# Kernel optimization log

Hardware: AMD Instinct MI355X
Metric: run time of the kernel (lower is better)

Reference implementation:

```python
import jax, jax.numpy as jnp
import numpy as np

N_NODES = 500000


def _gcn_conv(x, W, b, src, dst, n):
    # x: [N, Fin], W: [Fin, Fout]. PyG GCNConv with add_self_loops + sym norm.
    h = x @ W                                            # [N, Fout]
    deg = jax.ops.segment_sum(jnp.ones_like(dst, dtype=h.dtype), dst,
                              num_segments=n)            # in-degree incl self loops
    dinv = jnp.where(deg > 0, jax.lax.rsqrt(jnp.maximum(deg, 1)), 0.0)
    norm = dinv[src] * dinv[dst]                         # [E]
    msg = h[src] * norm[:, None]                         # gather + scale
    out = jax.ops.segment_sum(msg, dst, num_segments=n)  # scatter-add to targets
    return out + b


def setup_inputs() -> dict:
    key = jax.random.key(0)
    k1, k2, k3, k4 = jax.random.split(key, 4)
    x = jax.random.normal(k1, (N_NODES, 1), dtype=jnp.float32)
    edge_index = jax.random.randint(k2, (2, 8000000), 0, N_NODES, dtype=jnp.int64)
    W1 = jax.random.normal(k3, (1, 32), dtype=jnp.float32) * (1.0 / np.sqrt(1))
    b1 = jnp.zeros((32,), dtype=jnp.float32)
    W2 = jax.random.normal(k4, (32, 2), dtype=jnp.float32) * (1.0 / np.sqrt(32))
    b2 = jnp.zeros((2,), dtype=jnp.float32)
    return {"x": x, "edge_index": edge_index, "W1": W1, "b1": b1, "W2": W2, "b2": b2}


def reference(x, edge_index, W1, b1, W2, b2):
    n = x.shape[0]
    loops = jnp.arange(n, dtype=edge_index.dtype)
    src = jnp.concatenate([edge_index[0], loops])  # add self-loops
    dst = jnp.concatenate([edge_index[1], loops])
    h = _gcn_conv(x, W1, b1, src, dst, n)
    h = jax.nn.relu(h)
    # F.dropout(training=self.training): identity in eval mode
    h = _gcn_conv(h, W2, b2, src, dst, n)
    return jax.nn.log_softmax(h, axis=1)
```

## Files before the change

### kernel.cpp

```cpp
#include <hip/hip_runtime.h>


static constexpr int BKT_BITS = 11;
static constexpr int BKT = 1 << BKT_BITS;
static constexpr int NB = 256;
static constexpr int HB = 512;
static constexpr int HT = 256;
static constexpr int CHUNK = 8192;
static constexpr int SCT = 256;
static constexpr int PERT = CHUNK / SCT;

__global__ void __launch_bounds__(HT) k_hist(const int* __restrict__ dst, int e,
                                             int chunk, int nbkt,
                                             unsigned* __restrict__ totals) {
  __shared__ unsigned cnt[NB];
  for (int t = threadIdx.x; t < NB; t += HT) cnt[t] = 0;
  __syncthreads();
  int lo = blockIdx.x * chunk;
  int hi = min(lo + chunk, e);
  const int4* d4 = (const int4*)dst;
  for (int i = (lo >> 2) + threadIdx.x; i < (hi >> 2); i += HT) {
    int4 d = d4[i];
    atomicAdd(&cnt[((unsigned)d.x) >> BKT_BITS], 1u);
    atomicAdd(&cnt[((unsigned)d.y) >> BKT_BITS], 1u);
    atomicAdd(&cnt[((unsigned)d.z) >> BKT_BITS], 1u);
    atomicAdd(&cnt[((unsigned)d.w) >> BKT_BITS], 1u);
  }
  for (int i = ((hi >> 2) << 2) + threadIdx.x; i < hi; i += HT)
    atomicAdd(&cnt[((unsigned)dst[i]) >> BKT_BITS], 1u);
  __syncthreads();
  for (int t = threadIdx.x; t < nbkt; t += HT)
    if (cnt[t]) atomicAdd(&totals[t], cnt[t]);
}

__global__ void k_basescan(const unsigned* __restrict__ totals, int nbkt,
                           unsigned* __restrict__ gcur) {
  int lane = threadIdx.x;
  unsigned running = 0;
  for (int c = 0; c < NB; c += 64) {
    int k = c + lane;
    unsigned v = (k < nbkt) ? totals[k] : 0u;
    unsigned incl = v;
#pragma unroll
    for (int off = 1; off < 64; off <<= 1) {
      unsigned t = __shfl_up(incl, off);
      if (lane >= off) incl += t;
    }
    if (k < nbkt) gcur[k] = running + incl - v;
    running += __shfl(incl, 63);
  }
}

__global__ void __launch_bounds__(SCT) k_scatter(
    const int* __restrict__ src, const int* __restrict__ dst, int e, int nbkt,
    unsigned* __restrict__ gcur, unsigned* __restrict__ packed) {
  __shared__ unsigned staged[CHUNK];
  __shared__ unsigned cnt[NB];
  __shared__ unsigned cur[NB];
  __shared__ unsigned gseg[NB];
  __shared__ unsigned loff[NB + 1];
  const int tid = threadIdx.x;
  const int lo = blockIdx.x * CHUNK;
  for (int t = tid; t < NB; t += SCT) { cnt[t] = 0u; cur[t] = 0u; }
  __syncthreads();

  unsigned pk[PERT];
  unsigned bku[PERT / 4];
  const int4* s4 = (const int4*)src;
  const int4* d4 = (const int4*)dst;
#pragma unroll
  for (int jj = 0; jj < PERT / 4; ++jj) {
    int i4 = (lo >> 2) + jj * SCT + tid;
    unsigned b4 = 0xFFFFFFFFu;
    if (i4 * 4 + 3 < e) {
      int4 s = s4[i4];
      int4 d = d4[i4];
      unsigned k0 = ((unsigned)d.x) >> BKT_BITS, k1 = ((unsigned)d.y) >> BKT_BITS;
      unsigned k2 = ((unsigned)d.z) >> BKT_BITS, k3 = ((unsigned)d.w) >> BKT_BITS;
      pk[jj * 4 + 0] = ((unsigned)s.x << BKT_BITS) | ((unsigned)d.x & (BKT - 1));
      pk[jj * 4 + 1] = ((unsigned)s.y << BKT_BITS) | ((unsigned)d.y & (BKT - 1));
      pk[jj * 4 + 2] = ((unsigned)s.z << BKT_BITS) | ((unsigned)d.z & (BKT - 1));
      pk[jj * 4 + 3] = ((unsigned)s.w << BKT_BITS) | ((unsigned)d.w & (BKT - 1));
      b4 = k0 | (k1 << 8) | (k2 << 16) | (k3 << 24);
      atomicAdd(&cnt[k0], 1u);
      atomicAdd(&cnt[k1], 1u);
      atomicAdd(&cnt[k2], 1u);
      atomicAdd(&cnt[k3], 1u);
    } else {
#pragma unroll
      for (int c = 0; c < 4; ++c) {
        int i = i4 * 4 + c;
        if (i >= lo && i < e) {
          unsigned dd = (unsigned)dst[i];
          unsigned kk = dd >> BKT_BITS;
          pk[jj * 4 + c] = ((unsigned)src[i] << BKT_BITS) | (dd & (BKT - 1));
          b4 = (b4 & ~(0xFFu << (8 * c))) | (kk << (8 * c));
          atomicAdd(&cnt[kk], 1u);
        }
      }
    }
    bku[jj] = b4;
  }
  __syncthreads();

  if (tid < 64) {
    unsigned running = 0;
    for (int c = 0; c < NB; c += 64) {
      int k = c + tid;
      unsigned v = cnt[k];
      unsigned incl = v;
#pragma unroll
      for (int off = 1; off < 64; off <<= 1) {
        unsigned t = __shfl_up(incl, off);
        if (tid >= off) incl += t;
      }
      loff[k] = running + incl - v;
      running += __shfl(incl, 63);
    }
    if (tid == 0) loff[NB] = running;
  }
  __syncthreads();

  for (int k = tid; k < nbkt; k += SCT)
    if (cnt[k]) gseg[k] = atomicAdd(&gcur[k], cnt[k]);

#pragma unroll
  for (int jj = 0; jj < PERT / 4; ++jj) {
    unsigned b4 = bku[jj];
#pragma unroll
    for (int c = 0; c < 4; ++c) {
      unsigned k = (b4 >> (8 * c)) & 0xFFu;
      if (k != 0xFFu) {
        unsigned pos = loff[k] + atomicAdd(&cur[k], 1u);
        staged[pos] = pk[jj * 4 + c];
      }
    }
  }
  __syncthreads();

  int mv = (int)loff[nbkt];
  for (int t = tid; t < mv; t += SCT) {
    int a = 0, b = nbkt;
    while (b - a > 1) {
      int mid = (a + b) >> 1;
      if ((int)loff[mid] <= t) a = mid; else b = mid;
    }
    packed[gseg[a] + (unsigned)(t - (int)loff[a])] = staged[t];
  }
}

__global__ void __launch_bounds__(1024) k_degnode(
    const unsigned* __restrict__ packed, const unsigned* __restrict__ gcur,
    const float* __restrict__ x, int n, float* __restrict__ dinv,
    float* __restrict__ xs) {
  __shared__ unsigned cnt[BKT];
  int k = blockIdx.x;
  for (int t = threadIdx.x; t < BKT; t += blockDim.x) cnt[t] = 0;
  __syncthreads();
  unsigned lo = k ? gcur[k - 1] : 0u, hi = gcur[k];
  for (unsigned i = lo + threadIdx.x; i < hi; i += blockDim.x)
    atomicAdd(&cnt[packed[i] & (BKT - 1)], 1u);
  __syncthreads();
  int g0 = k << BKT_BITS;
  for (int t = threadIdx.x; t < BKT; t += blockDim.x) {
    int g = g0 + t;
    if (g < n) {
      float di = rsqrtf((float)(cnt[t] + 1u));
      dinv[g] = di;
      xs[g] = di * x[g];
    }
  }
}

__global__ void __launch_bounds__(1024) k_accA2(
    const unsigned* __restrict__ packed, const unsigned* __restrict__ gcur,
    const float* __restrict__ dinv, const float* __restrict__ xs,
    const float* __restrict__ W1, const float* __restrict__ b1,
    const float* __restrict__ W2, int n, float2* __restrict__ yd) {
  __shared__ float acc[BKT];
  __shared__ float sW1[32], sb1[32], sW2[64];
  if (threadIdx.x < 32) {
    sW1[threadIdx.x] = W1[threadIdx.x];
    sb1[threadIdx.x] = b1[threadIdx.x];
  } else if (threadIdx.x < 96) {
    sW2[threadIdx.x - 32] = W2[threadIdx.x - 32];
  }
  for (int t = threadIdx.x; t < BKT; t += blockDim.x) acc[t] = 0.0f;
  __syncthreads();
  int k = blockIdx.x;
  unsigned lo = k ? gcur[k - 1] : 0u, hi = gcur[k];
  for (unsigned i = lo + threadIdx.x; i < hi; i += blockDim.x) {
    unsigned p = packed[i];
    atomicAdd(&acc[p & (BKT - 1)], xs[p >> BKT_BITS]);
  }
  __syncthreads();
  int g0 = k << BKT_BITS;
  for (int t = threadIdx.x; t < BKT; t += blockDim.x) {
    int g = g0 + t;
    if (g >= n) continue;
    float di = dinv[g];
    float s = di * (acc[t] + xs[g]);
    float y0 = 0.0f, y1 = 0.0f;
#pragma unroll
    for (int f = 0; f < 32; ++f) {
      float h = fmaxf(fmaf(s, sW1[f], sb1[f]), 0.0f);
      y0 = fmaf(h, sW2[2 * f + 0], y0);
      y1 = fmaf(h, sW2[2 * f + 1], y1);
    }
    yd[g] = make_float2(di * y0, di * y1);
  }
}

__global__ void __launch_bounds__(1024) k_accB3(
    const unsigned* __restrict__ packed, const unsigned* __restrict__ gcur,
    const float* __restrict__ dinv, const float2* __restrict__ yd,
    const float* __restrict__ b2, int n, float2* __restrict__ out) {
  __shared__ float a0[BKT], a1[BKT];
  for (int t = threadIdx.x; t < BKT; t += blockDim.x) {
    a0[t] = 0.0f;
    a1[t] = 0.0f;
  }
  __syncthreads();
  int k = blockIdx.x;
  unsigned lo = k ? gcur[k - 1] : 0u, hi = gcur[k];
  for (unsigned i = lo + threadIdx.x; i < hi; i += blockDim.x) {
    unsigned p = packed[i];
    float2 v = yd[p >> BKT_BITS];
    unsigned l = p & (BKT - 1);
    atomicAdd(&a0[l], v.x);
    atomicAdd(&a1[l], v.y);
  }
  __syncthreads();
  float b20 = b2[0], b21 = b2[1];
  int g0 = k << BKT_BITS;
  for (int t = threadIdx.x; t < BKT; t += blockDim.x) {
    int g = g0 + t;
    if (g >= n) continue;
    float di = dinv[g];
    float2 yv = yd[g];
    float t0 = fmaf(di, a0[t] + yv.x, b2[0] * 0.0f + b20);
    float t1 = fmaf(di, a1[t] + yv.y, b21);
    float m = fmaxf(t0, t1);
    float l2 = m + logf(expf(t0 - m) + expf(t1 - m));
    out[g] = make_float2(t0 - l2, t1 - l2);
  }
}

extern "C" void kernel_launch(void* const* d_in, const int* in_sizes, int n_in,
                              void* d_out, int out_size, void* d_ws, size_t ws_size,
                              hipStream_t stream) {
  const float* x = (const float*)d_in[0];
  const int* edge = (const int*)d_in[1];
  const float* W1 = (const float*)d_in[2];
  const float* b1 = (const float*)d_in[3];
  const float* W2 = (const float*)d_in[4];
  const float* b2 = (const float*)d_in[5];
  float2* out = (float2*)d_out;

  const int n = in_sizes[0];
  const int e = in_sizes[1] / 2;
  const int* src = edge;
  const int* dst = edge + e;

  const int nbkt = (n + BKT - 1) >> BKT_BITS;
  const int hchunk = (((e + HB - 1) / HB) + 3) & ~3;
  const int sgrid = (e + CHUNK - 1) / CHUNK;

  char* ws = (char*)d_ws;
  unsigned* packed = (unsigned*)ws;
  unsigned* totals = (unsigned*)(ws + (size_t)e * 4);
  unsigned* gcur = totals + NB;
  float* dinv = (float*)(gcur + NB);
  float* xs = dinv + n;
  float2* yd = (float2*)(xs + n);

  hipMemsetAsync(totals, 0, NB * sizeof(unsigned), stream);
  k_hist<<<HB, HT, 0, stream>>>(dst, e, hchunk, nbkt, totals);
  k_basescan<<<1, 64, 0, stream>>>(totals, nbkt, gcur);
  k_scatter<<<sgrid, SCT, 0, stream>>>(src, dst, e, nbkt, gcur, packed);
  k_degnode<<<nbkt, 1024, 0, stream>>>(packed, gcur, x, n, dinv, xs);
  k_accA2<<<nbkt, 1024, 0, stream>>>(packed, gcur, dinv, xs, W1, b1, W2, n, yd);
  k_accB3<<<nbkt, 1024, 0, stream>>>(packed, gcur, dinv, yd, b2, n, out);
}
```

Before: 236.3 us.

## Split per-bucket accumulation across multiple blocks with partial sums and node kernels

Each destination bucket's edge range is now divided into S slices, each handled by a 256-thread block that writes a partial accumulator array to workspace. Separate per-node kernels then sum the partials and apply the dense MLP or log-softmax. The aim is more blocks per bucket, since about 245 buckets underfill the GPU's CUs. Loads are unrolled 4x, and nontemporal loads and stores are added on the packed edge stream. The cost is two extra launches plus workspace traffic for the partials, and S depends on the available workspace size.

```diff
diff --git a/kernel.cpp b/kernel.cpp
--- a/kernel.cpp
+++ b/kernel.cpp
@@ -9,6 +9,7 @@
 static constexpr int CHUNK = 8192;
 static constexpr int SCT = 256;
 static constexpr int PERT = CHUNK / SCT;
+static constexpr int AT = 256;
 
 __global__ void __launch_bounds__(HT) k_hist(const int* __restrict__ dst, int e,
                                              int chunk, int nbkt,
@@ -145,7 +146,8 @@
       int mid = (a + b) >> 1;
       if ((int)loff[mid] <= t) a = mid; else b = mid;
     }
-    packed[gseg[a] + (unsigned)(t - (int)loff[a])] = staged[t];
+    __builtin_nontemporal_store(staged[t],
+                                packed + gseg[a] + (unsigned)(t - (int)loff[a]));
   }
 }
 
@@ -155,14 +157,24 @@
     float* __restrict__ xs) {
   __shared__ unsigned cnt[BKT];
   int k = blockIdx.x;
-  for (int t = threadIdx.x; t < BKT; t += blockDim.x) cnt[t] = 0;
+  for (int t = threadIdx.x; t < BKT; t += 1024) cnt[t] = 0;
   __syncthreads();
   unsigned lo = k ? gcur[k - 1] : 0u, hi = gcur[k];
-  for (unsigned i = lo + threadIdx.x; i < hi; i += blockDim.x)
-    atomicAdd(&cnt[packed[i] & (BKT - 1)], 1u);
+  unsigned i = lo + threadIdx.x;
+  for (; i + 3u * 1024u < hi; i += 4096u) {
+    unsigned p0 = __builtin_nontemporal_load(packed + i);
+    unsigned p1 = __builtin_nontemporal_load(packed + i + 1024);
+    unsigned p2 = __builtin_nontemporal_load(packed + i + 2048);
+    unsigned p3 = __builtin_nontemporal_load(packed + i + 3072);
+    atomicAdd(&cnt[p0 & (BKT - 1)], 1u);
+    atomicAdd(&cnt[p1 & (BKT - 1)], 1u);
+    atomicAdd(&cnt[p2 & (BKT - 1)], 1u);
+    atomicAdd(&cnt[p3 & (BKT - 1)], 1u);
+  }
+  for (; i < hi; i += 1024u) atomicAdd(&cnt[packed[i] & (BKT - 1)], 1u);
   __syncthreads();
   int g0 = k << BKT_BITS;
-  for (int t = threadIdx.x; t < BKT; t += blockDim.x) {
+  for (int t = threadIdx.x; t < BKT; t += 1024) {
     int g = g0 + t;
     if (g < n) {
       float di = rsqrtf((float)(cnt[t] + 1u));
@@ -172,12 +184,49 @@
   }
 }
 
-__global__ void __launch_bounds__(1024) k_accA2(
+__global__ void __launch_bounds__(AT) k_accA_part(
     const unsigned* __restrict__ packed, const unsigned* __restrict__ gcur,
-    const float* __restrict__ dinv, const float* __restrict__ xs,
-    const float* __restrict__ W1, const float* __restrict__ b1,
-    const float* __restrict__ W2, int n, float2* __restrict__ yd) {
+    const float* __restrict__ xs, int S, float* __restrict__ pA) {
   __shared__ float acc[BKT];
+  int k = blockIdx.x / S, s = blockIdx.x - k * S;
+  for (int t = threadIdx.x; t < BKT; t += AT) acc[t] = 0.0f;
+  __syncthreads();
+  unsigned blo = k ? gcur[k - 1] : 0u, bhi = gcur[k];
+  unsigned slice = (bhi - blo + S - 1) / S;
+  unsigned lo = blo + s * slice;
+  unsigned hi = lo + slice;
+  if (hi > bhi) hi = bhi;
+  if (lo > bhi) lo = bhi;
+  unsigned i = lo + threadIdx.x;
+  for (; i + 3u * AT < hi; i += 4u * AT) {
+    unsigned p0 = __builtin_nontemporal_load(packed + i);
+    unsigned p1 = __builtin_nontemporal_load(packed + i + AT);
+    unsigned p2 = __builtin_nontemporal_load(packed + i + 2 * AT);
+    unsigned p3 = __builtin_nontemporal_load(packed + i + 3 * AT);
+    float v0 = xs[p0 >> BKT_BITS];
+    float v1 = xs[p1 >> BKT_BITS];
+    float v2 = xs[p2 >> BKT_BITS];
+    float v3 = xs[p3 >> BKT_BITS];
+    atomicAdd(&acc[p0 & (BKT - 1)], v0);
+    atomicAdd(&acc[p1 & (BKT - 1)], v1);
+    atomicAdd(&acc[p2 & (BKT - 1)], v2);
+    atomicAdd(&acc[p3 & (BKT - 1)], v3);
+  }
+  for (; i < hi; i += AT) {
+    unsigned p = packed[i];
+    atomicAdd(&acc[p & (BKT - 1)], xs[p >> BKT_BITS]);
+  }
+  __syncthreads();
+  float* dstp = pA + ((size_t)(k * S + s) << BKT_BITS);
+  for (int t = threadIdx.x; t < BKT; t += AT)
+    __builtin_nontemporal_store(acc[t], dstp + t);
+}
+
+__global__ void __launch_bounds__(256) k_nodeA(
+    const float* __restrict__ pA, const float* __restrict__ dinv,
+    const float* __restrict__ xs, const float* __restrict__ W1,
+    const float* __restrict__ b1, const float* __restrict__ W2, int S, int n,
+    float2* __restrict__ yd) {
   __shared__ float sW1[32], sb1[32], sW2[64];
   if (threadIdx.x < 32) {
     sW1[threadIdx.x] = W1[threadIdx.x];
@@ -185,65 +234,87 @@
   } else if (threadIdx.x < 96) {
     sW2[threadIdx.x - 32] = W2[threadIdx.x - 32];
   }
-  for (int t = threadIdx.x; t < BKT; t += blockDim.x) acc[t] = 0.0f;
-  __syncthreads();
-  int k = blockIdx.x;
-  unsigned lo = k ? gcur[k - 1] : 0u, hi = gcur[k];
-  for (unsigned i = lo + threadIdx.x; i < hi; i += blockDim.x) {
-    unsigned p = packed[i];
-    atomicAdd(&acc[p & (BKT - 1)], xs[p >> BKT_BITS]);
-  }
-  __syncthreads();
-  int g0 = k << BKT_BITS;
-  for (int t = threadIdx.x; t < BKT; t += blockDim.x) {
-    int g = g0 + t;
-    if (g >= n) continue;
-    float di = dinv[g];
-    float s = di * (acc[t] + xs[g]);
-    float y0 = 0.0f, y1 = 0.0f;
-#pragma unroll
-    for (int f = 0; f < 32; ++f) {
-      float h = fmaxf(fmaf(s, sW1[f], sb1[f]), 0.0f);
-      y0 = fmaf(h, sW2[2 * f + 0], y0);
-      y1 = fmaf(h, sW2[2 * f + 1], y1);
-    }
-    yd[g] = make_float2(di * y0, di * y1);
-  }
-}
-
-__global__ void __launch_bounds__(1024) k_accB3(
+  __syncthreads();
+  int g = blockIdx.x * 256 + threadIdx.x;
+  if (g >= n) return;
+  int k = g >> BKT_BITS, t = g & (BKT - 1);
+  float a = 0.0f;
+  for (int s = 0; s < S; ++s) a += pA[((size_t)(k * S + s) << BKT_BITS) + t];
+  float di = dinv[g];
+  float sv = di * (a + xs[g]);
+  float y0 = 0.0f, y1 = 0.0f;
+#pragma unroll
+  for (int f = 0; f < 32; ++f) {
+    float h = fmaxf(fmaf(sv, sW1[f], sb1[f]), 0.0f);
+    y0 = fmaf(h, sW2[2 * f + 0], y0);
+    y1 = fmaf(h, sW2[2 * f + 1], y1);
+  }
+  yd[g] = make_float2(di * y0, di * y1);
+}
+
+__global__ void __launch_bounds__(AT) k_accB_part(
     const unsigned* __restrict__ packed, const unsigned* __restrict__ gcur,
-    const float* __restrict__ dinv, const float2* __restrict__ yd,
-    const float* __restrict__ b2, int n, float2* __restrict__ out) {
-  __shared__ float a0[BKT], a1[BKT];
-  for (int t = threadIdx.x; t < BKT; t += blockDim.x) {
-    a0[t] = 0.0f;
-    a1[t] = 0.0f;
-  }
-  __syncthreads();
-  int k = blockIdx.x;
-  unsigned lo = k ? gcur[k - 1] : 0u, hi = gcur[k];
-  for (unsigned i = lo + threadIdx.x; i < hi; i += blockDim.x) {
+    const float2* __restrict__ yd, int S, float2* __restrict__ pB) {
+  __shared__ float2 av[BKT];
+  int k = blockIdx.x / S, s = blockIdx.x - k * S;
+  for (int t = threadIdx.x; t < BKT; t += AT) av[t] = make_float2(0.0f, 0.0f);
+  __syncthreads();
+  unsigned blo = k ? gcur[k - 1] : 0u, bhi = gcur[k];
+  unsigned slice = (bhi - blo + S - 1) / S;
+  unsigned lo = blo + s * slice;
+  unsigned hi = lo + slice;
+  if (hi > bhi) hi = bhi;
+  if (lo > bhi) lo = bhi;
+  unsigned i = lo + threadIdx.x;
+  for (; i + 3u * AT < hi; i += 4u * AT) {
+    unsigned p0 = __builtin_nontemporal_load(packed + i);
+    unsigned p1 = __builtin_nontemporal_load(packed + i + AT);
+    unsigned p2 = __builtin_nontemporal_load(packed + i + 2 * AT);
+    unsigned p3 = __builtin_nontemporal_load(packed + i + 3 * AT);
+    float2 v0 = yd[p0 >> BKT_BITS];
+    float2 v1 = yd[p1 >> BKT_BITS];
+    float2 v2 = yd[p2 >> BKT_BITS];
+    float2 v3 = yd[p3 >> BKT_BITS];
+    atomicAdd(&av[p0 & (BKT - 1)].x, v0.x);
+    atomicAdd(&av[p0 & (BKT - 1)].y, v0.y);
+    atomicAdd(&av[p1 & (BKT - 1)].x, v1.x);
+    atomicAdd(&av[p1 & (BKT - 1)].y, v1.y);
+    atomicAdd(&av[p2 & (BKT - 1)].x, v2.x);
+    atomicAdd(&av[p2 & (BKT - 1)].y, v2.y);
+    atomicAdd(&av[p3 & (BKT - 1)].x, v3.x);
+    atomicAdd(&av[p3 & (BKT - 1)].y, v3.y);
+  }
+  for (; i < hi; i += AT) {
     unsigned p = packed[i];
     float2 v = yd[p >> BKT_BITS];
-    unsigned l = p & (BKT - 1);
-    atomicAdd(&a0[l], v.x);
-    atomicAdd(&a1[l], v.y);
-  }
-  __syncthreads();
-  float b20 = b2[0], b21 = b2[1];
-  int g0 = k << BKT_BITS;
-  for (int t = threadIdx.x; t < BKT; t += blockDim.x) {
-    int g = g0 + t;
-    if (g >= n) continue;
-    float di = dinv[g];
-    float2 yv = yd[g];
-    float t0 = fmaf(di, a0[t] + yv.x, b2[0] * 0.0f + b20);
-    float t1 = fmaf(di, a1[t] + yv.y, b21);
-    float m = fmaxf(t0, t1);
-    float l2 = m + logf(expf(t0 - m) + expf(t1 - m));
-    out[g] = make_float2(t0 - l2, t1 - l2);
-  }
+    atomicAdd(&av[p & (BKT - 1)].x, v.x);
+    atomicAdd(&av[p & (BKT - 1)].y, v.y);
+  }
+  __syncthreads();
+  float2* dstp = pB + ((size_t)(k * S + s) << BKT_BITS);
+  for (int t = threadIdx.x; t < BKT; t += AT) dstp[t] = av[t];
+}
+
+__global__ void __launch_bounds__(256) k_nodeB(
+    const float2* __restrict__ pB, const float* __restrict__ dinv,
+    const float2* __restrict__ yd, const float* __restrict__ b2, int S, int n,
+    float2* __restrict__ out) {
+  int g = blockIdx.x * 256 + threadIdx.x;
+  if (g >= n) return;
+  int k = g >> BKT_BITS, t = g & (BKT - 1);
+  float s0 = 0.0f, s1 = 0.0f;
+  for (int s = 0; s < S; ++s) {
+    float2 v = pB[((size_t)(k * S + s) << BKT_BITS) + t];
+    s0 += v.x;
+    s1 += v.y;
+  }
+  float di = dinv[g];
+  float2 yv = yd[g];
+  float t0 = fmaf(di, s0 + yv.x, b2[0]);
+  float t1 = fmaf(di, s1 + yv.y, b2[1]);
+  float m = fmaxf(t0, t1);
+  float l = m + logf(expf(t0 - m) + expf(t1 - m));
+  out[g] = make_float2(t0 - l, t1 - l);
 }
 
 extern "C" void kernel_launch(void* const* d_in, const int* in_sizes, int n_in,
@@ -265,20 +336,31 @@
   const int nbkt = (n + BKT - 1) >> BKT_BITS;
   const int hchunk = (((e + HB - 1) / HB) + 3) & ~3;
   const int sgrid = (e + CHUNK - 1) / CHUNK;
+  const int ngrid = (n + 255) / 256;
 
   char* ws = (char*)d_ws;
-  unsigned* packed = (unsigned*)ws;
-  unsigned* totals = (unsigned*)(ws + (size_t)e * 4);
-  unsigned* gcur = totals + NB;
-  float* dinv = (float*)(gcur + NB);
-  float* xs = dinv + n;
-  float2* yd = (float2*)(xs + n);
+  size_t off = 0;
+  unsigned* packed = (unsigned*)(ws + off); off += (size_t)e * 4;
+  unsigned* totals = (unsigned*)(ws + off); off += NB * 4;
+  unsigned* gcur = (unsigned*)(ws + off);   off += NB * 4;
+  float* dinv = (float*)(ws + off);         off += (size_t)n * 4;
+  float* xs = (float*)(ws + off);           off += (size_t)n * 4;
+  float2* yd = (float2*)(ws + off);         off += (size_t)n * 8;
+  size_t rem = (ws_size > off) ? ws_size - off : 0;
+  int SA = (int)(rem / ((size_t)nbkt * BKT * 4));
+  int SB = (int)(rem / ((size_t)nbkt * BKT * 8));
+  SA = SA < 1 ? 1 : (SA > 8 ? 8 : SA);
+  SB = SB < 1 ? 1 : (SB > 8 ? 8 : SB);
+  float* pA = (float*)(ws + off);
+  float2* pB = (float2*)(ws + off);
 
   hipMemsetAsync(totals, 0, NB * sizeof(unsigned), stream);
   k_hist<<<HB, HT, 0, stream>>>(dst, e, hchunk, nbkt, totals);
   k_basescan<<<1, 64, 0, stream>>>(totals, nbkt, gcur);
   k_scatter<<<sgrid, SCT, 0, stream>>>(src, dst, e, nbkt, gcur, packed);
   k_degnode<<<nbkt, 1024, 0, stream>>>(packed, gcur, x, n, dinv, xs);
-  k_accA2<<<nbkt, 1024, 0, stream>>>(packed, gcur, dinv, xs, W1, b1, W2, n, yd);
-  k_accB3<<<nbkt, 1024, 0, stream>>>(packed, gcur, dinv, yd, b2, n, out);
-}
+  k_accA_part<<<nbkt * SA, AT, 0, stream>>>(packed, gcur, xs, SA, pA);
+  k_nodeA<<<ngrid, 256, 0, stream>>>(pA, dinv, xs, W1, b1, W2, SA, n, yd);
+  k_accB_part<<<nbkt * SB, AT, 0, stream>>>(packed, gcur, yd, SB, pB);
+  k_nodeB<<<ngrid, 256, 0, stream>>>(pB, dinv, yd, b2, SB, n, out);
+}
```

New measurement: 247.4 us. 1.05x slower.

## Sub-bin edges by source range with deterministic per-chunk scan offsets

Applied to the files above, without the earlier changes.

The bucketing of edges now uses a 2D bin (destination bucket × source range of 65536), so within each destination bucket the edges are ordered by source block. This should improve locality of the xs/yd gathers in the aggregation kernels. Global atomics for segment allocation are replaced by a per-chunk histogram, a column scan and a bin scan. The aggregation kernels also switch to 128-bit nontemporal loads of the packed edges, and the scatter uses nontemporal stores. The cost is a larger histogram workspace, an extra scan pass (nbin blocks), and more LDS per scatter block, which may lower occupancy.

```diff
diff --git a/kernel.cpp b/kernel.cpp
--- a/kernel.cpp
+++ b/kernel.cpp
@@ -3,109 +3,141 @@
 
 static constexpr int BKT_BITS = 11;
 static constexpr int BKT = 1 << BKT_BITS;
-static constexpr int NB = 256;
-static constexpr int HB = 512;
-static constexpr int HT = 256;
+static constexpr int SRC_SH = 16;
+static constexpr int NBIN_MAX = 2048;
 static constexpr int CHUNK = 8192;
 static constexpr int SCT = 256;
 static constexpr int PERT = CHUNK / SCT;
 
-__global__ void __launch_bounds__(HT) k_hist(const int* __restrict__ dst, int e,
-                                             int chunk, int nbkt,
-                                             unsigned* __restrict__ totals) {
-  __shared__ unsigned cnt[NB];
-  for (int t = threadIdx.x; t < NB; t += HT) cnt[t] = 0;
-  __syncthreads();
-  int lo = blockIdx.x * chunk;
-  int hi = min(lo + chunk, e);
+using u32x4 = __attribute__((ext_vector_type(4))) unsigned;
+
+__global__ void __launch_bounds__(SCT) k_hist(const int* __restrict__ src,
+                                              const int* __restrict__ dst, int e,
+                                              int nbin, int C,
+                                              unsigned* __restrict__ hist) {
+  __shared__ unsigned cnt[NBIN_MAX];
+  for (int t = threadIdx.x; t < NBIN_MAX; t += SCT) cnt[t] = 0;
+  __syncthreads();
+  int lo = blockIdx.x * CHUNK;
+  int hi = min(lo + CHUNK, e);
+  const int4* s4 = (const int4*)src;
   const int4* d4 = (const int4*)dst;
-  for (int i = (lo >> 2) + threadIdx.x; i < (hi >> 2); i += HT) {
+  for (int i = (lo >> 2) + threadIdx.x; i < (hi >> 2); i += SCT) {
+    int4 s = s4[i];
     int4 d = d4[i];
-    atomicAdd(&cnt[((unsigned)d.x) >> BKT_BITS], 1u);
-    atomicAdd(&cnt[((unsigned)d.y) >> BKT_BITS], 1u);
-    atomicAdd(&cnt[((unsigned)d.z) >> BKT_BITS], 1u);
-    atomicAdd(&cnt[((unsigned)d.w) >> BKT_BITS], 1u);
-  }
-  for (int i = ((hi >> 2) << 2) + threadIdx.x; i < hi; i += HT)
-    atomicAdd(&cnt[((unsigned)dst[i]) >> BKT_BITS], 1u);
-  __syncthreads();
-  for (int t = threadIdx.x; t < nbkt; t += HT)
-    if (cnt[t]) atomicAdd(&totals[t], cnt[t]);
-}
-
-__global__ void k_basescan(const unsigned* __restrict__ totals, int nbkt,
-                           unsigned* __restrict__ gcur) {
+    atomicAdd(&cnt[(((unsigned)d.x) >> BKT_BITS) * C + (((unsigned)s.x) >> SRC_SH)], 1u);
+    atomicAdd(&cnt[(((unsigned)d.y) >> BKT_BITS) * C + (((unsigned)s.y) >> SRC_SH)], 1u);
+    atomicAdd(&cnt[(((unsigned)d.z) >> BKT_BITS) * C + (((unsigned)s.z) >> SRC_SH)], 1u);
+    atomicAdd(&cnt[(((unsigned)d.w) >> BKT_BITS) * C + (((unsigned)s.w) >> SRC_SH)], 1u);
+  }
+  for (int i = ((hi >> 2) << 2) + threadIdx.x; i < hi; i += SCT)
+    atomicAdd(&cnt[(((unsigned)dst[i]) >> BKT_BITS) * C + (((unsigned)src[i]) >> SRC_SH)], 1u);
+  __syncthreads();
+  unsigned* hrow = hist + (size_t)blockIdx.x * nbin;
+  for (int t = threadIdx.x; t < nbin; t += SCT) hrow[t] = cnt[t];
+}
+
+__global__ void k_colscan(const unsigned* __restrict__ hist, int sgrid, int nbin,
+                          unsigned* __restrict__ colpre,
+                          unsigned* __restrict__ totals) {
+  int k = blockIdx.x;
   int lane = threadIdx.x;
   unsigned running = 0;
-  for (int c = 0; c < NB; c += 64) {
-    int k = c + lane;
-    unsigned v = (k < nbkt) ? totals[k] : 0u;
+  int rounds = (sgrid + 63) >> 6;
+  for (int c = 0; c < rounds; ++c) {
+    int b = c * 64 + lane;
+    unsigned v = (b < sgrid) ? hist[(size_t)b * nbin + k] : 0u;
     unsigned incl = v;
 #pragma unroll
     for (int off = 1; off < 64; off <<= 1) {
       unsigned t = __shfl_up(incl, off);
       if (lane >= off) incl += t;
     }
-    if (k < nbkt) gcur[k] = running + incl - v;
+    if (b < sgrid) colpre[(size_t)b * nbin + k] = running + incl - v;
     running += __shfl(incl, 63);
   }
+  if (lane == 0) totals[k] = running;
+}
+
+__global__ void k_binscan(const unsigned* __restrict__ totals, int nbin,
+                          unsigned* __restrict__ base) {
+  int lane = threadIdx.x;
+  unsigned running = 0;
+  for (int c = 0; c < NBIN_MAX; c += 64) {
+    int k = c + lane;
+    unsigned v = (k < nbin) ? totals[k] : 0u;
+    unsigned incl = v;
+#pragma unroll
+    for (int off = 1; off < 64; off <<= 1) {
+      unsigned t = __shfl_up(incl, off);
+      if (lane >= off) incl += t;
+    }
+    if (k < nbin) base[k] = running + incl - v;
+    running += __shfl(incl, 63);
+  }
+  if (lane == 0) base[nbin] = running;
 }
 
 __global__ void __launch_bounds__(SCT) k_scatter(
-    const int* __restrict__ src, const int* __restrict__ dst, int e, int nbkt,
-    unsigned* __restrict__ gcur, unsigned* __restrict__ packed) {
+    const int* __restrict__ src, const int* __restrict__ dst, int e, int nbin,
+    int C, const unsigned* __restrict__ colpre, const unsigned* __restrict__ base,
+    unsigned* __restrict__ packed) {
   __shared__ unsigned staged[CHUNK];
-  __shared__ unsigned cnt[NB];
-  __shared__ unsigned cur[NB];
-  __shared__ unsigned gseg[NB];
-  __shared__ unsigned loff[NB + 1];
+  __shared__ unsigned cnt[NBIN_MAX];
+  __shared__ unsigned loff[NBIN_MAX + 1];
+  __shared__ unsigned gbase[NBIN_MAX];
   const int tid = threadIdx.x;
   const int lo = blockIdx.x * CHUNK;
-  for (int t = tid; t < NB; t += SCT) { cnt[t] = 0u; cur[t] = 0u; }
+  for (int t = tid; t < NBIN_MAX; t += SCT) cnt[t] = 0u;
   __syncthreads();
 
   unsigned pk[PERT];
-  unsigned bku[PERT / 4];
+  unsigned short bin[PERT];
   const int4* s4 = (const int4*)src;
   const int4* d4 = (const int4*)dst;
 #pragma unroll
   for (int jj = 0; jj < PERT / 4; ++jj) {
     int i4 = (lo >> 2) + jj * SCT + tid;
-    unsigned b4 = 0xFFFFFFFFu;
     if (i4 * 4 + 3 < e) {
       int4 s = s4[i4];
       int4 d = d4[i4];
-      unsigned k0 = ((unsigned)d.x) >> BKT_BITS, k1 = ((unsigned)d.y) >> BKT_BITS;
-      unsigned k2 = ((unsigned)d.z) >> BKT_BITS, k3 = ((unsigned)d.w) >> BKT_BITS;
+      unsigned b0 = (((unsigned)d.x) >> BKT_BITS) * C + (((unsigned)s.x) >> SRC_SH);
+      unsigned b1 = (((unsigned)d.y) >> BKT_BITS) * C + (((unsigned)s.y) >> SRC_SH);
+      unsigned b2 = (((unsigned)d.z) >> BKT_BITS) * C + (((unsigned)s.z) >> SRC_SH);
+      unsigned b3 = (((unsigned)d.w) >> BKT_BITS) * C + (((unsigned)s.w) >> SRC_SH);
       pk[jj * 4 + 0] = ((unsigned)s.x << BKT_BITS) | ((unsigned)d.x & (BKT - 1));
       pk[jj * 4 + 1] = ((unsigned)s.y << BKT_BITS) | ((unsigned)d.y & (BKT - 1));
       pk[jj * 4 + 2] = ((unsigned)s.z << BKT_BITS) | ((unsigned)d.z & (BKT - 1));
       pk[jj * 4 + 3] = ((unsigned)s.w << BKT_BITS) | ((unsigned)d.w & (BKT - 1));
-      b4 = k0 | (k1 << 8) | (k2 << 16) | (k3 << 24);
-      atomicAdd(&cnt[k0], 1u);
-      atomicAdd(&cnt[k1], 1u);
-      atomicAdd(&cnt[k2], 1u);
-      atomicAdd(&cnt[k3], 1u);
+      bin[jj * 4 + 0] = (unsigned short)b0;
+      bin[jj * 4 + 1] = (unsigned short)b1;
+      bin[jj * 4 + 2] = (unsigned short)b2;
+      bin[jj * 4 + 3] = (unsigned short)b3;
+      atomicAdd(&cnt[b0], 1u);
+      atomicAdd(&cnt[b1], 1u);
+      atomicAdd(&cnt[b2], 1u);
+      atomicAdd(&cnt[b3], 1u);
     } else {
 #pragma unroll
       for (int c = 0; c < 4; ++c) {
         int i = i4 * 4 + c;
+        bin[jj * 4 + c] = 0xFFFFu;
         if (i >= lo && i < e) {
+          unsigned ss = (unsigned)src[i];
           unsigned dd = (unsigned)dst[i];
-          unsigned kk = dd >> BKT_BITS;
-          pk[jj * 4 + c] = ((unsigned)src[i] << BKT_BITS) | (dd & (BKT - 1));
-          b4 = (b4 & ~(0xFFu << (8 * c))) | (kk << (8 * c));
-          atomicAdd(&cnt[kk], 1u);
+          unsigned bb = (dd >> BKT_BITS) * C + (ss >> SRC_SH);
+          pk[jj * 4 + c] = (ss << BKT_BITS) | (dd & (BKT - 1));
+          bin[jj * 4 + c] = (unsigned short)bb;
+          atomicAdd(&cnt[bb], 1u);
         }
       }
     }
-    bku[jj] = b4;
   }
   __syncthreads();
 
   if (tid < 64) {
     unsigned running = 0;
-    for (int c = 0; c < NB; c += 64) {
+    for (int c = 0; c < NBIN_MAX; c += 64) {
       int k = c + tid;
       unsigned v = cnt[k];
       unsigned incl = v;
@@ -117,52 +149,66 @@
       loff[k] = running + incl - v;
       running += __shfl(incl, 63);
     }
-    if (tid == 0) loff[NB] = running;
-  }
-  __syncthreads();
-
-  for (int k = tid; k < nbkt; k += SCT)
-    if (cnt[k]) gseg[k] = atomicAdd(&gcur[k], cnt[k]);
-
-#pragma unroll
-  for (int jj = 0; jj < PERT / 4; ++jj) {
-    unsigned b4 = bku[jj];
-#pragma unroll
-    for (int c = 0; c < 4; ++c) {
-      unsigned k = (b4 >> (8 * c)) & 0xFFu;
-      if (k != 0xFFu) {
-        unsigned pos = loff[k] + atomicAdd(&cur[k], 1u);
-        staged[pos] = pk[jj * 4 + c];
-      }
-    }
-  }
-  __syncthreads();
-
-  int mv = (int)loff[nbkt];
+    if (tid == 0) loff[NBIN_MAX] = running;
+  }
+  __syncthreads();
+  const unsigned* cp = colpre + (size_t)blockIdx.x * nbin;
+  for (int t = tid; t < NBIN_MAX; t += SCT) {
+    cnt[t] = 0u;
+    if (t < nbin) gbase[t] = base[t] + cp[t];
+  }
+  __syncthreads();
+
+#pragma unroll
+  for (int jj = 0; jj < PERT; ++jj) {
+    unsigned b = bin[jj];
+    if (b != 0xFFFFu) {
+      unsigned pos = loff[b] + atomicAdd(&cnt[b], 1u);
+      staged[pos] = pk[jj];
+    }
+  }
+  __syncthreads();
+
+  int mv = (int)loff[NBIN_MAX];
   for (int t = tid; t < mv; t += SCT) {
-    int a = 0, b = nbkt;
+    int a = 0, b = nbin;
     while (b - a > 1) {
       int mid = (a + b) >> 1;
       if ((int)loff[mid] <= t) a = mid; else b = mid;
     }
-    packed[gseg[a] + (unsigned)(t - (int)loff[a])] = staged[t];
+    __builtin_nontemporal_store(staged[t],
+                                packed + gbase[a] + (unsigned)(t - (int)loff[a]));
   }
 }
 
 __global__ void __launch_bounds__(1024) k_degnode(
-    const unsigned* __restrict__ packed, const unsigned* __restrict__ gcur,
+    const unsigned* __restrict__ packed, const unsigned* __restrict__ base, int C,
     const float* __restrict__ x, int n, float* __restrict__ dinv,
     float* __restrict__ xs) {
   __shared__ unsigned cnt[BKT];
   int k = blockIdx.x;
-  for (int t = threadIdx.x; t < BKT; t += blockDim.x) cnt[t] = 0;
-  __syncthreads();
-  unsigned lo = k ? gcur[k - 1] : 0u, hi = gcur[k];
-  for (unsigned i = lo + threadIdx.x; i < hi; i += blockDim.x)
+  for (int t = threadIdx.x; t < BKT; t += 1024) cnt[t] = 0;
+  __syncthreads();
+  unsigned lo = base[k * C], hi = base[(k + 1) * C];
+  unsigned loA = (lo + 3u) & ~3u;
+  unsigned hiA = hi & ~3u;
+  if (loA > hi) loA = hi;
+  if (hiA < loA) hiA = loA;
+  for (unsigned i = lo + threadIdx.x; i < loA; i += 1024)
     atomicAdd(&cnt[packed[i] & (BKT - 1)], 1u);
+  for (unsigned i = hiA + threadIdx.x; i < hi; i += 1024)
+    atomicAdd(&cnt[packed[i] & (BKT - 1)], 1u);
+  const u32x4* p4 = (const u32x4*)packed;
+  for (unsigned q = (loA >> 2) + threadIdx.x; q < (hiA >> 2); q += 1024) {
+    u32x4 p = __builtin_nontemporal_load(p4 + q);
+    atomicAdd(&cnt[p.x & (BKT - 1)], 1u);
+    atomicAdd(&cnt[p.y & (BKT - 1)], 1u);
+    atomicAdd(&cnt[p.z & (BKT - 1)], 1u);
+    atomicAdd(&cnt[p.w & (BKT - 1)], 1u);
+  }
   __syncthreads();
   int g0 = k << BKT_BITS;
-  for (int t = threadIdx.x; t < BKT; t += blockDim.x) {
+  for (int t = threadIdx.x; t < BKT; t += 1024) {
     int g = g0 + t;
     if (g < n) {
       float di = rsqrtf((float)(cnt[t] + 1u));
@@ -173,7 +219,7 @@
 }
 
 __global__ void __launch_bounds__(1024) k_accA2(
-    const unsigned* __restrict__ packed, const unsigned* __restrict__ gcur,
+    const unsigned* __restrict__ packed, const unsigned* __restrict__ base, int C,
     const float* __restrict__ dinv, const float* __restrict__ xs,
     const float* __restrict__ W1, const float* __restrict__ b1,
     const float* __restrict__ W2, int n, float2* __restrict__ yd) {
@@ -185,17 +231,37 @@
   } else if (threadIdx.x < 96) {
     sW2[threadIdx.x - 32] = W2[threadIdx.x - 32];
   }
-  for (int t = threadIdx.x; t < BKT; t += blockDim.x) acc[t] = 0.0f;
+  for (int t = threadIdx.x; t < BKT; t += 1024) acc[t] = 0.0f;
   __syncthreads();
   int k = blockIdx.x;
-  unsigned lo = k ? gcur[k - 1] : 0u, hi = gcur[k];
-  for (unsigned i = lo + threadIdx.x; i < hi; i += blockDim.x) {
+  unsigned lo = base[k * C], hi = base[(k + 1) * C];
+  unsigned loA = (lo + 3u) & ~3u;
+  unsigned hiA = hi & ~3u;
+  if (loA > hi) loA = hi;
+  if (hiA < loA) hiA = loA;
+  for (unsigned i = lo + threadIdx.x; i < loA; i += 1024) {
     unsigned p = packed[i];
     atomicAdd(&acc[p & (BKT - 1)], xs[p >> BKT_BITS]);
   }
+  for (unsigned i = hiA + threadIdx.x; i < hi; i += 1024) {
+    unsigned p = packed[i];
+    atomicAdd(&acc[p & (BKT - 1)], xs[p >> BKT_BITS]);
+  }
+  const u32x4* p4 = (const u32x4*)packed;
+  for (unsigned q = (loA >> 2) + threadIdx.x; q < (hiA >> 2); q += 1024) {
+    u32x4 p = __builtin_nontemporal_load(p4 + q);
+    float v0 = xs[p.x >> BKT_BITS];
+    float v1 = xs[p.y >> BKT_BITS];
+    float v2 = xs[p.z >> BKT_BITS];
+    float v3 = xs[p.w >> BKT_BITS];
+    atomicAdd(&acc[p.x & (BKT - 1)], v0);
+    atomicAdd(&acc[p.y & (BKT - 1)], v1);
+    atomicAdd(&acc[p.z & (BKT - 1)], v2);
+    atomicAdd(&acc[p.w & (BKT - 1)], v3);
+  }
   __syncthreads();
   int g0 = k << BKT_BITS;
-  for (int t = threadIdx.x; t < BKT; t += blockDim.x) {
+  for (int t = threadIdx.x; t < BKT; t += 1024) {
     int g = g0 + t;
     if (g >= n) continue;
     float di = dinv[g];
@@ -212,37 +278,62 @@
 }
 
 __global__ void __launch_bounds__(1024) k_accB3(
-    const unsigned* __restrict__ packed, const unsigned* __restrict__ gcur,
+    const unsigned* __restrict__ packed, const unsigned* __restrict__ base, int C,
     const float* __restrict__ dinv, const float2* __restrict__ yd,
     const float* __restrict__ b2, int n, float2* __restrict__ out) {
   __shared__ float a0[BKT], a1[BKT];
-  for (int t = threadIdx.x; t < BKT; t += blockDim.x) {
+  for (int t = threadIdx.x; t < BKT; t += 1024) {
     a0[t] = 0.0f;
     a1[t] = 0.0f;
   }
   __syncthreads();
   int k = blockIdx.x;
-  unsigned lo = k ? gcur[k - 1] : 0u, hi = gcur[k];
-  for (unsigned i = lo + threadIdx.x; i < hi; i += blockDim.x) {
+  unsigned lo = base[k * C], hi = base[(k + 1) * C];
+  unsigned loA = (lo + 3u) & ~3u;
+  unsigned hiA = hi & ~3u;
+  if (loA > hi) loA = hi;
+  if (hiA < loA) hiA = loA;
+  for (unsigned i = lo + threadIdx.x; i < loA; i += 1024) {
     unsigned p = packed[i];
     float2 v = yd[p >> BKT_BITS];
-    unsigned l = p & (BKT - 1);
-    atomicAdd(&a0[l], v.x);
-    atomicAdd(&a1[l], v.y);
+    atomicAdd(&a0[p & (BKT - 1)], v.x);
+    atomicAdd(&a1[p & (BKT - 1)], v.y);
+  }
+  for (unsigned i = hiA + threadIdx.x; i < hi; i += 1024) {
+    unsigned p = packed[i];
+    float2 v = yd[p >> BKT_BITS];
+    atomicAdd(&a0[p & (BKT - 1)], v.x);
+    atomicAdd(&a1[p & (BKT - 1)], v.y);
+  }
+  const u32x4* p4 = (const u32x4*)packed;
+  for (unsigned q = (loA >> 2) + threadIdx.x; q < (hiA >> 2); q += 1024) {
+    u32x4 p = __builtin_nontemporal_load(p4 + q);
+    float2 v0 = yd[p.x >> BKT_BITS];
+    float2 v1 = yd[p.y >> BKT_BITS];
+    float2 v2 = yd[p.z >> BKT_BITS];
+    float2 v3 = yd[p.w >> BKT_BITS];
+    atomicAdd(&a0[p.x & (BKT - 1)], v0.x);
+    atomicAdd(&a1[p.x & (BKT - 1)], v0.y);
+    atomicAdd(&a0[p.y & (BKT - 1)], v1.x);
+    atomicAdd(&a1[p.y & (BKT - 1)], v1.y);
+    atomicAdd(&a0[p.z & (BKT - 1)], v2.x);
+    atomicAdd(&a1[p.z & (BKT - 1)], v2.y);
+    atomicAdd(&a0[p.w & (BKT - 1)], v3.x);
+    atomicAdd(&a1[p.w & (BKT - 1)], v3.y);
   }
   __syncthreads();
   float b20 = b2[0], b21 = b2[1];
   int g0 = k << BKT_BITS;
-  for (int t = threadIdx.x; t < BKT; t += blockDim.x) {
+  for (int t = threadIdx.x; t < BKT; t += 1024) {
     int g = g0 + t;
     if (g >= n) continue;
     float di = dinv[g];
     float2 yv = yd[g];
-    float t0 = fmaf(di, a0[t] + yv.x, b2[0] * 0.0f + b20);
+    float t0 = fmaf(di, a0[t] + yv.x, b20);
     float t1 = fmaf(di, a1[t] + yv.y, b21);
     float m = fmaxf(t0, t1);
-    float l2 = m + logf(expf(t0 - m) + expf(t1 - m));
-    out[g] = make_float2(t0 - l2, t1 - l2);
+    float l = m + logf(expf(t0 - m) + expf(t1 - m));
+    out[g] = make_float2(t0 - l, t1 - l);
   }
 }
 
@@ -263,22 +354,26 @@
   const int* dst = edge + e;
 
   const int nbkt = (n + BKT - 1) >> BKT_BITS;
-  const int hchunk = (((e + HB - 1) / HB) + 3) & ~3;
+  const int C = (n + 65535) >> SRC_SH;
+  const int nbin = nbkt * C;
   const int sgrid = (e + CHUNK - 1) / CHUNK;
 
   char* ws = (char*)d_ws;
-  unsigned* packed = (unsigned*)ws;
-  unsigned* totals = (unsigned*)(ws + (size_t)e * 4);
-  unsigned* gcur = totals + NB;
-  float* dinv = (float*)(gcur + NB);
-  float* xs = dinv + n;
-  float2* yd = (float2*)(xs + n);
-
-  hipMemsetAsync(totals, 0, NB * sizeof(unsigned), stream);
-  k_hist<<<HB, HT, 0, stream>>>(dst, e, hchunk, nbkt, totals);
-  k_basescan<<<1, 64, 0, stream>>>(totals, nbkt, gcur);
-  k_scatter<<<sgrid, SCT, 0, stream>>>(src, dst, e, nbkt, gcur, packed);
-  k_degnode<<<nbkt, 1024, 0, stream>>>(packed, gcur, x, n, dinv, xs);
-  k_accA2<<<nbkt, 1024, 0, stream>>>(packed, gcur, dinv, xs, W1, b1, W2, n, yd);
-  k_accB3<<<nbkt, 1024, 0, stream>>>(packed, gcur, dinv, yd, b2, n, out);
-}
+  size_t off = 0;
+  unsigned* packed = (unsigned*)(ws + off); off += (size_t)e * 4;
+  unsigned* base = (unsigned*)(ws + off);   off += (NBIN_MAX + 2) * 4;
+  unsigned* totals = (unsigned*)(ws + off); off += NBIN_MAX * 4;
+  float* dinv = (float*)(ws + off);         off += (size_t)n * 4;
+  float* xs = (float*)(ws + off);           off += (size_t)n * 4;
+  float2* yd = (float2*)(ws + off);         off += (size_t)n * 8;
+  unsigned* hist = (unsigned*)(ws + off);   off += (size_t)sgrid * nbin * 4;
+  unsigned* colpre = (unsigned*)(ws + off); off += (size_t)sgrid * nbin * 4;
+
+  k_hist<<<sgrid, SCT, 0, stream>>>(src, dst, e, nbin, C, hist);
+  k_colscan<<<nbin, 64, 0, stream>>>(hist, sgrid, nbin, colpre, totals);
+  k_binscan<<<1, 64, 0, stream>>>(totals, nbin, base);
+  k_scatter<<<sgrid, SCT, 0, stream>>>(src, dst, e, nbin, C, colpre, base, packed);
+  k_degnode<<<nbkt, 1024, 0, stream>>>(packed, base, C, x, n, dinv, xs);
+  k_accA2<<<nbkt, 1024, 0, stream>>>(packed, base, C, dinv, xs, W1, b1, W2, n, yd);
+  k_accB3<<<nbkt, 1024, 0, stream>>>(packed, base, C, dinv, yd, b2, n, out);
+}
```

After: 314.5 us. 33.1% more time.

## Sort each bucket's edges by source class to improve gather locality

Applied to the files above, without the earlier changes.

Replaces the degree kernel with a per-bucket counting sort that orders packed edges by the top bits of the source index (8 classes, per-wave offsets), writing a second packed array. The two accumulation passes then gather xs/yd from more localized source ranges, and they now read packed edges as 128-bit nontemporal loads with 4 gathers in flight. The scatter also uses nontemporal stores. The cost is an extra full read and write of the edge array plus more shared atomics in the sort kernel, and loff[NB] replaces loff[nbkt] as the move count.

```diff
diff --git a/kernel.cpp b/kernel.cpp
--- a/kernel.cpp
+++ b/kernel.cpp
@@ -9,6 +9,11 @@
 static constexpr int CHUNK = 8192;
 static constexpr int SCT = 256;
 static constexpr int PERT = CHUNK / SCT;
+static constexpr int CLS_SH = 27;
+static constexpr int NCLS = 8;
+static constexpr int NW = 16;
+
+using u32x4 = __attribute__((ext_vector_type(4))) unsigned;
 
 __global__ void __launch_bounds__(HT) k_hist(const int* __restrict__ dst, int e,
                                              int chunk, int nbkt,
@@ -138,34 +143,105 @@
   }
   __syncthreads();
 
-  int mv = (int)loff[nbkt];
+  int mv = (int)loff[NB];
   for (int t = tid; t < mv; t += SCT) {
     int a = 0, b = nbkt;
     while (b - a > 1) {
       int mid = (a + b) >> 1;
       if ((int)loff[mid] <= t) a = mid; else b = mid;
     }
-    packed[gseg[a] + (unsigned)(t - (int)loff[a])] = staged[t];
-  }
-}
-
-__global__ void __launch_bounds__(1024) k_degnode(
+    __builtin_nontemporal_store(staged[t],
+                                packed + gseg[a] + (unsigned)(t - (int)loff[a]));
+  }
+}
+
+__global__ void __launch_bounds__(1024) k_classort(
     const unsigned* __restrict__ packed, const unsigned* __restrict__ gcur,
-    const float* __restrict__ x, int n, float* __restrict__ dinv,
-    float* __restrict__ xs) {
-  __shared__ unsigned cnt[BKT];
-  int k = blockIdx.x;
-  for (int t = threadIdx.x; t < BKT; t += blockDim.x) cnt[t] = 0;
+    const float* __restrict__ x, int n, unsigned* __restrict__ packed2,
+    float* __restrict__ dinv, float* __restrict__ xs) {
+  __shared__ unsigned cnt_node[BKT];
+  __shared__ unsigned wcnt[NCLS * NW];
+  __shared__ unsigned wcur[NCLS * NW];
+  const int k = blockIdx.x;
+  const int tid = threadIdx.x;
+  const int w = tid >> 6;
+  for (int t = tid; t < BKT; t += 1024) cnt_node[t] = 0;
+  if (tid < NCLS * NW) wcnt[tid] = 0;
   __syncthreads();
   unsigned lo = k ? gcur[k - 1] : 0u, hi = gcur[k];
-  for (unsigned i = lo + threadIdx.x; i < hi; i += blockDim.x)
-    atomicAdd(&cnt[packed[i] & (BKT - 1)], 1u);
-  __syncthreads();
+  unsigned loA = (lo + 3u) & ~3u, hiA = hi & ~3u;
+  if (loA > hi) loA = hi;
+  if (hiA < loA) hiA = loA;
+
+  for (unsigned i = lo + tid; i < loA; i += 1024) {
+    unsigned p = packed[i];
+    atomicAdd(&cnt_node[p & (BKT - 1)], 1u);
+    atomicAdd(&wcnt[(p >> CLS_SH) * NW + w], 1u);
+  }
+  for (unsigned i = hiA + tid; i < hi; i += 1024) {
+    unsigned p = packed[i];
+    atomicAdd(&cnt_node[p & (BKT - 1)], 1u);
+    atomicAdd(&wcnt[(p >> CLS_SH) * NW + w], 1u);
+  }
+  const u32x4* p4 = (const u32x4*)packed;
+  for (unsigned q = (loA >> 2) + tid; q < (hiA >> 2); q += 1024) {
+    u32x4 p = p4[q];
+    atomicAdd(&cnt_node[p.x & (BKT - 1)], 1u);
+    atomicAdd(&wcnt[(p.x >> CLS_SH) * NW + w], 1u);
+    atomicAdd(&cnt_node[p.y & (BKT - 1)], 1u);
+    atomicAdd(&wcnt[(p.y >> CLS_SH) * NW + w], 1u);
+    atomicAdd(&cnt_node[p.z & (BKT - 1)], 1u);
+    atomicAdd(&wcnt[(p.z >> CLS_SH) * NW + w], 1u);
+    atomicAdd(&cnt_node[p.w & (BKT - 1)], 1u);
+    atomicAdd(&wcnt[(p.w >> CLS_SH) * NW + w], 1u);
+  }
+  __syncthreads();
+
+  if (tid < 64) {
+    unsigned running = 0;
+#pragma unroll
+    for (int r = 0; r < (NCLS * NW) / 64; ++r) {
+      int idx = r * 64 + tid;
+      unsigned v = wcnt[idx];
+      unsigned incl = v;
+#pragma unroll
+      for (int off = 1; off < 64; off <<= 1) {
+        unsigned t = __shfl_up(incl, off);
+        if (tid >= off) incl += t;
+      }
+      wcur[idx] = running + incl - v;
+      running += __shfl(incl, 63);
+    }
+  }
+  __syncthreads();
+
+  for (unsigned i = lo + tid; i < loA; i += 1024) {
+    unsigned p = packed[i];
+    unsigned pos = atomicAdd(&wcur[(p >> CLS_SH) * NW + w], 1u);
+    packed2[lo + pos] = p;
+  }
+  for (unsigned i = hiA + tid; i < hi; i += 1024) {
+    unsigned p = packed[i];
+    unsigned pos = atomicAdd(&wcur[(p >> CLS_SH) * NW + w], 1u);
+    packed2[lo + pos] = p;
+  }
+  for (unsigned q = (loA >> 2) + tid; q < (hiA >> 2); q += 1024) {
+    u32x4 p = p4[q];
+    unsigned pos0 = atomicAdd(&wcur[(p.x >> CLS_SH) * NW + w], 1u);
+    packed2[lo + pos0] = p.x;
+    unsigned pos1 = atomicAdd(&wcur[(p.y >> CLS_SH) * NW + w], 1u);
+    packed2[lo + pos1] = p.y;
+    unsigned pos2 = atomicAdd(&wcur[(p.z >> CLS_SH) * NW + w], 1u);
+    packed2[lo + pos2] = p.z;
+    unsigned pos3 = atomicAdd(&wcur[(p.w >> CLS_SH) * NW + w], 1u);
+    packed2[lo + pos3] = p.w;
+  }
+
   int g0 = k << BKT_BITS;
-  for (int t = threadIdx.x; t < BKT; t += blockDim.x) {
+  for (int t = tid; t < BKT; t += 1024) {
     int g = g0 + t;
     if (g < n) {
-      float di = rsqrtf((float)(cnt[t] + 1u));
+      float di = rsqrtf((float)(cnt_node[t] + 1u));
       dinv[g] = di;
       xs[g] = di * x[g];
     }
@@ -173,7 +249,7 @@
 }
 
 __global__ void __launch_bounds__(1024) k_accA2(
-    const unsigned* __restrict__ packed, const unsigned* __restrict__ gcur,
+    const unsigned* __restrict__ packed2, const unsigned* __restrict__ gcur,
     const float* __restrict__ dinv, const float* __restrict__ xs,
     const float* __restrict__ W1, const float* __restrict__ b1,
     const float* __restrict__ W2, int n, float2* __restrict__ yd) {
@@ -185,17 +261,36 @@
   } else if (threadIdx.x < 96) {
     sW2[threadIdx.x - 32] = W2[threadIdx.x - 32];
   }
-  for (int t = threadIdx.x; t < BKT; t += blockDim.x) acc[t] = 0.0f;
+  for (int t = threadIdx.x; t < BKT; t += 1024) acc[t] = 0.0f;
   __syncthreads();
   int k = blockIdx.x;
   unsigned lo = k ? gcur[k - 1] : 0u, hi = gcur[k];
-  for (unsigned i = lo + threadIdx.x; i < hi; i += blockDim.x) {
-    unsigned p = packed[i];
+  unsigned loA = (lo + 3u) & ~3u, hiA = hi & ~3u;
+  if (loA > hi) loA = hi;
+  if (hiA < loA) hiA = loA;
+  for (unsigned i = lo + threadIdx.x; i < loA; i += 1024) {
+    unsigned p = packed2[i];
     atomicAdd(&acc[p & (BKT - 1)], xs[p >> BKT_BITS]);
   }
+  for (unsigned i = hiA + threadIdx.x; i < hi; i += 1024) {
+    unsigned p = packed2[i];
+    atomicAdd(&acc[p & (BKT - 1)], xs[p >> BKT_BITS]);
+  }
+  const u32x4* p4 = (const u32x4*)packed2;
+  for (unsigned q = (loA >> 2) + threadIdx.x; q < (hiA >> 2); q += 1024) {
+    u32x4 p = __builtin_nontemporal_load(p4 + q);
+    float v0 = xs[p.x >> BKT_BITS];
+    float v1 = xs[p.y >> BKT_BITS];
+    float v2 = xs[p.z >> BKT_BITS];
+    float v3 = xs[p.w >> BKT_BITS];
+    atomicAdd(&acc[p.x & (BKT - 1)], v0);
+    atomicAdd(&acc[p.y & (BKT - 1)], v1);
+    atomicAdd(&acc[p.z & (BKT - 1)], v2);
+    atomicAdd(&acc[p.w & (BKT - 1)], v3);
+  }
   __syncthreads();
   int g0 = k << BKT_BITS;
-  for (int t = threadIdx.x; t < BKT; t += blockDim.x) {
+  for (int t = threadIdx.x; t < BKT; t += 1024) {
     int g = g0 + t;
     if (g >= n) continue;
     float di = dinv[g];
@@ -212,37 +307,61 @@
 }
 
 __global__ void __launch_bounds__(1024) k_accB3(
-    const unsigned* __restrict__ packed, const unsigned* __restrict__ gcur,
+    const unsigned* __restrict__ packed2, const unsigned* __restrict__ gcur,
     const float* __restrict__ dinv, const float2* __restrict__ yd,
     const float* __restrict__ b2, int n, float2* __restrict__ out) {
   __shared__ float a0[BKT], a1[BKT];
-  for (int t = threadIdx.x; t < BKT; t += blockDim.x) {
+  for (int t = threadIdx.x; t < BKT; t += 1024) {
     a0[t] = 0.0f;
     a1[t] = 0.0f;
   }
   __syncthreads();
   int k = blockIdx.x;
   unsigned lo = k ? gcur[k - 1] : 0u, hi = gcur[k];
-  for (unsigned i = lo + threadIdx.x; i < hi; i += blockDim.x) {
-    unsigned p = packed[i];
+  unsigned loA = (lo + 3u) & ~3u, hiA = hi & ~3u;
+  if (loA > hi) loA = hi;
+  if (hiA < loA) hiA = loA;
+  for (unsigned i = lo + threadIdx.x; i < loA; i += 1024) {
+    unsigned p = packed2[i];
     float2 v = yd[p >> BKT_BITS];
-    unsigned l = p & (BKT - 1);
-    atomicAdd(&a0[l], v.x);
-    atomicAdd(&a1[l], v.y);
+    atomicAdd(&a0[p & (BKT - 1)], v.x);
+    atomicAdd(&a1[p & (BKT - 1)], v.y);
+  }
+  for (unsigned i = hiA + threadIdx.x; i < hi; i += 1024) {
+    unsigned p = packed2[i];
+    float2 v = yd[p >> BKT_BITS];
+    atomicAdd(&a0[p & (BKT - 1)], v.x);
+    atomicAdd(&a1[p & (BKT - 1)], v.y);
+  }
+  const u32x4* p4 = (const u32x4*)packed2;
+  for (unsigned q = (loA >> 2) + threadIdx.x; q < (hiA >> 2); q += 1024) {
+    u32x4 p = __builtin_nontemporal_load(p4 + q);
+    float2 v0 = yd[p.x >> BKT_BITS];
+    float2 v1 = yd[p.y >> BKT_BITS];
+    float2 v2 = yd[p.z >> BKT_BITS];
+    float2 v3 = yd[p.w >> BKT_BITS];
+    atomicAdd(&a0[p.x & (BKT - 1)], v0.x);
+    atomicAdd(&a1[p.x & (BKT - 1)], v0.y);
+    atomicAdd(&a0[p.y & (BKT - 1)], v1.x);
+    atomicAdd(&a1[p.y & (BKT - 1)], v1.y);
+    atomicAdd(&a0[p.z & (BKT - 1)], v2.x);
+    atomicAdd(&a1[p.z & (BKT - 1)], v2.y);
+    atomicAdd(&a0[p.w & (BKT - 1)], v3.x);
+    atomicAdd(&a1[p.w & (BKT - 1)], v3.y);
   }
   __syncthreads();
   float b20 = b2[0], b21 = b2[1];
   int g0 = k << BKT_BITS;
-  for (int t = threadIdx.x; t < BKT; t += blockDim.x) {
+  for (int t = threadIdx.x; t < BKT; t += 1024) {
     int g = g0 + t;
     if (g >= n) continue;
     float di = dinv[g];
     float2 yv = yd[g];
-    float t0 = fmaf(di, a0[t] + yv.x, b2[0] * 0.0f + b20);
+    float t0 = fmaf(di, a0[t] + yv.x, b20);
     float t1 = fmaf(di, a1[t] + yv.y, b21);
     float m = fmaxf(t0, t1);
-    float l2 = m + logf(expf(t0 - m) + expf(t1 - m));
-    out[g] = make_float2(t0 - l2, t1 - l2);
+    float l = m + logf(expf(t0 - m) + expf(t1 - m));
+    out[g] = make_float2(t0 - l, t1 - l);
   }
 }
 
@@ -267,18 +386,20 @@
   const int sgrid = (e + CHUNK - 1) / CHUNK;
 
   char* ws = (char*)d_ws;
-  unsigned* packed = (unsigned*)ws;
-  unsigned* totals = (unsigned*)(ws + (size_t)e * 4);
-  unsigned* gcur = totals + NB;
-  float* dinv = (float*)(gcur + NB);
-  float* xs = dinv + n;
-  float2* yd = (float2*)(xs + n);
+  size_t off = 0;
+  unsigned* packed = (unsigned*)(ws + off);  off += (size_t)e * 4;
+  unsigned* packed2 = (unsigned*)(ws + off); off += (size_t)e * 4;
+  unsigned* totals = (unsigned*)(ws + off);  off += NB * 4;
+  unsigned* gcur = (unsigned*)(ws + off);    off += NB * 4;
+  float* dinv = (float*)(ws + off);          off += (size_t)n * 4;
+  float* xs = (float*)(ws + off);            off += (size_t)n * 4;
+  float2* yd = (float2*)(ws + off);          off += (size_t)n * 8;
 
   hipMemsetAsync(totals, 0, NB * sizeof(unsigned), stream);
   k_hist<<<HB, HT, 0, stream>>>(dst, e, hchunk, nbkt, totals);
   k_basescan<<<1, 64, 0, stream>>>(totals, nbkt, gcur);
   k_scatter<<<sgrid, SCT, 0, stream>>>(src, dst, e, nbkt, gcur, packed);
-  k_degnode<<<nbkt, 1024, 0, stream>>>(packed, gcur, x, n, dinv, xs);
-  k_accA2<<<nbkt, 1024, 0, stream>>>(packed, gcur, dinv, xs, W1, b1, W2, n, yd);
-  k_accB3<<<nbkt, 1024, 0, stream>>>(packed, gcur, dinv, yd, b2, n, out);
-}
+  k_classort<<<nbkt, 1024, 0, stream>>>(packed, gcur, x, n, packed2, dinv, xs);
+  k_accA2<<<nbkt, 1024, 0, stream>>>(packed2, gcur, dinv, xs, W1, b1, W2, n, yd);
+  k_accB3<<<nbkt, 1024, 0, stream>>>(packed2, gcur, dinv, yd, b2, n, out);
+}
```

Result: slower. 253.9 us (+7.4%).
